# Kernel optimization log

Measured on AMD Instinct MI355X. Metric: run time of the kernel, lower is better.

The kernel has to match this reference:

```python
import jax, jax.numpy as jnp
import numpy as np

N_HEADS, INPUT_DIM, EMBED_DIM = 8, 512, 512
KEY_DIM = EMBED_DIM // N_HEADS  # val_dim == key_dim == 64


def _uniform(key, shape, stdv):
    return jax.random.uniform(key, shape, jnp.float32, -stdv, stdv)


def setup_inputs() -> dict:
    key = jax.random.key(0)
    kh, kq, kk, kv, ko = jax.random.split(key, 5)
    stdv_qkv = 1.0 / np.sqrt(KEY_DIM)
    stdv_out = 1.0 / np.sqrt(EMBED_DIM)
    return {
        "h": jax.random.normal(kh, (4, 2048, INPUT_DIM), jnp.float32),
        "W_query": _uniform(kq, (N_HEADS, INPUT_DIM, KEY_DIM), stdv_qkv),
        "W_key": _uniform(kk, (N_HEADS, INPUT_DIM, KEY_DIM), stdv_qkv),
        "W_val": _uniform(kv, (N_HEADS, INPUT_DIM, KEY_DIM), stdv_qkv),
        "W_out": _uniform(ko, (N_HEADS * KEY_DIM, EMBED_DIM), stdv_out),
    }


def reference(h, W_query, W_key, W_val, W_out):
    # h: [b, n, d_in]; W_{q,k,v}: [H, d_in, dk]; W_out: [H*dk, d_model]
    norm = 1.0 / np.sqrt(KEY_DIM)
    Q = jnp.einsum('bnd,hdk->hbnk', h, W_query)
    K = jnp.einsum('bnd,hdk->hbnk', h, W_key)
    V = jnp.einsum('bnd,hdk->hbnk', h, W_val)
    compat = norm * jnp.einsum('hbnk,hbmk->hbnm', Q, K)  # [H,b,n,n]
    attn = jax.nn.softmax(compat, axis=-1)
    heads = jnp.einsum('hbnm,hbmk->hbnk', attn, V)        # [H,b,n,dk]
    b, n = h.shape[0], h.shape[1]
    heads = jnp.transpose(heads, (1, 2, 0, 3)).reshape(b, n, N_HEADS * KEY_DIM)
    return heads @ W_out
```

## Files before the change

### kernel.cpp

```cpp
#include <hip/hip_runtime.h>
#include <hip/hip_bf16.h>
#include <hip/hip_fp16.h>

#define H 8
#define B 4
#define NSEQ 2048
#define DIN 512
#define DK 64
#define DMODEL 512
#define ROWS (B*NSEQ)

typedef _Float16 f16x8 __attribute__((ext_vector_type(8)));
typedef _Float16 f16x4 __attribute__((ext_vector_type(4)));
typedef float f32x4 __attribute__((ext_vector_type(4)));

#define EXP2F(x) __builtin_amdgcn_exp2f(x)

#define AS1(p) ((const __attribute__((address_space(1))) void*)(const void*)(p))
#define AS3(p) ((__attribute__((address_space(3))) void*)(void*)(p))

__global__ void k_prep(const float* __restrict__ h,
                       const float* __restrict__ Wq,
                       const float* __restrict__ Wk,
                       const float* __restrict__ Wv,
                       const float* __restrict__ Wo,
                       _Float16* __restrict__ hb,
                       _Float16* __restrict__ Wt,
                       _Float16* __restrict__ Wot)
{
    const long nh = (long)ROWS * DIN;
    const long nw = (long)3 * H * DK * DIN;
    const long no = (long)DMODEL * DMODEL;
    const long total = nh + nw + no;
    for (long i = (long)blockIdx.x * blockDim.x + threadIdx.x; i < total;
         i += (long)gridDim.x * blockDim.x) {
        if (i < nh) {
            hb[i] = (_Float16)h[i];
        } else if (i < nh + nw) {
            int j = (int)(i - nh);
            int m   = j / (H * DK * DIN);
            int rem = j % (H * DK * DIN);
            int hh  = rem / (DK * DIN);
            int r2  = rem % (DK * DIN);
            int c   = r2 / DIN;
            int d   = r2 % DIN;
            const float* W = (m == 0) ? Wq : ((m == 1) ? Wk : Wv);
            Wt[j] = (_Float16)W[hh * DIN * DK + d * DK + c];
        } else {
            int j = (int)(i - nh - nw);
            int e = j / DMODEL;
            int c = j % DMODEL;
            Wot[j] = (_Float16)Wo[c * DMODEL + e];
        }
    }
}

__global__ __launch_bounds__(256, 4) void k_qkv(
    const _Float16* __restrict__ hb,
    const _Float16* __restrict__ Wt,
    _Float16* __restrict__ Qs,
    _Float16* __restrict__ Kb,
    _Float16* __restrict__ Vt)
{
    const int rt = blockIdx.x;
    const int ct = blockIdx.y;
    const int t  = threadIdx.x;
    const int w  = t >> 6;
    const int l  = t & 63;
    const int l15 = l & 15, lg = l >> 4;
    const int wr = w >> 1, wc = w & 1;

    __shared__ _Float16 Al[2][128*32];
    __shared__ _Float16 Bl[2][128*32];

    const int srow  = l >> 2;
    const int schnk = (l & 3) ^ (srow & 3);
    const _Float16* asrc = hb + (long)(rt*128 + w*16 + srow)*DIN + schnk*8;
    const _Float16* bsrc = Wt + (long)(ct*128 + w*16 + srow)*DIN + schnk*8;

    auto stage = [&](int kt, int bufi) {
        const _Float16* as = asrc + kt*32;
        const _Float16* bs = bsrc + kt*32;
        __builtin_amdgcn_global_load_lds(AS1(as),          AS3(&Al[bufi][w*512]),        16, 0, 0);
        __builtin_amdgcn_global_load_lds(AS1(as + 64*DIN), AS3(&Al[bufi][2048 + w*512]), 16, 0, 0);
        __builtin_amdgcn_global_load_lds(AS1(bs),          AS3(&Bl[bufi][w*512]),        16, 0, 0);
        __builtin_amdgcn_global_load_lds(AS1(bs + 64*DIN), AS3(&Bl[bufi][2048 + w*512]), 16, 0, 0);
    };

    f32x4 acc[4][4] = {};

    stage(0, 0);
    __syncthreads();

    const int co = (lg ^ (l15 & 3)) * 8;
    for (int kt = 0; kt < 16; ++kt) {
        const int cur = kt & 1;
        if (kt + 1 < 16) stage(kt + 1, cur ^ 1);

        f16x8 af[4], bf[4];
#pragma unroll
        for (int am = 0; am < 4; ++am)
            af[am] = *(const f16x8*)&Al[cur][(wr*64 + am*16 + l15)*32 + co];
#pragma unroll
        for (int an = 0; an < 4; ++an)
            bf[an] = *(const f16x8*)&Bl[cur][(wc*64 + an*16 + l15)*32 + co];
#pragma unroll
        for (int am = 0; am < 4; ++am)
#pragma unroll
            for (int an = 0; an < 4; ++an)
                acc[am][an] = __builtin_amdgcn_mfma_f32_16x16x32_f16(af[am], bf[an], acc[am][an], 0, 0, 0);

        __syncthreads();
    }

    const int m = (ct*128) >> 9;
    const float QSCALE = 0.125f * 1.44269504088896f;
#pragma unroll
    for (int an = 0; an < 4; ++an) {
        const int col = ct*128 + wc*64 + an*16 + l15;
        const int hd = (col >> 6) & 7, dk = col & 63;
#pragma unroll
        for (int am = 0; am < 4; ++am) {
            const int rowb = rt*128 + wr*64 + am*16 + lg*4;
            const int b = rowb >> 11, n = rowb & 2047;
            const long p = (long)hd*B + b;
            if (m == 0) {
#pragma unroll
                for (int r = 0; r < 4; ++r)
                    Qs[(p*NSEQ + n + r)*DK + dk] = (_Float16)(acc[am][an][r] * QSCALE);
            } else if (m == 1) {
#pragma unroll
                for (int r = 0; r < 4; ++r)
                    Kb[(p*NSEQ + n + r)*DK + dk] = (_Float16)acc[am][an][r];
            } else {
                f16x4 pk;
                pk[0] = (_Float16)acc[am][an][0]; pk[1] = (_Float16)acc[am][an][1];
                pk[2] = (_Float16)acc[am][an][2]; pk[3] = (_Float16)acc[am][an][3];
                *(f16x4*)&Vt[(p*DK + dk)*NSEQ + n] = pk;
            }
        }
    }
}

__global__ __launch_bounds__(256, 2) void k_attn(
    const _Float16* __restrict__ Qs,
    const _Float16* __restrict__ Kb,
    const _Float16* __restrict__ Vt,
    _Float16* __restrict__ heads)
{
    const int bid = blockIdx.x;
    const int xcd = bid & 7, slot = bid >> 3;
    const int p   = (xcd << 2) | (slot >> 4);
    const int qt  = slot & 15;
    const int t = threadIdx.x, w = t >> 6, l = t & 63;
    const int l15 = l & 15, lg = l >> 4;

    __shared__ _Float16 Kl[2][64][64];
    __shared__ _Float16 Vl[2][64][64];
    __shared__ _Float16 Plds[4][2][16][64];

    const _Float16* Qp = Qs + (long)p*NSEQ*DK;
    const _Float16* Kp = Kb + (long)p*NSEQ*DK;
    const _Float16* Vp = Vt + (long)p*DK*NSEQ;

    const int qrow = qt*128 + w*32;
    f16x8 qa[2][2];
#pragma unroll
    for (int G = 0; G < 2; ++G) {
        qa[G][0] = *(const f16x8*)(Qp + (long)(qrow + G*16 + l15)*DK + 8*lg);
        qa[G][1] = *(const f16x8*)(Qp + (long)(qrow + G*16 + l15)*DK + 32 + 8*lg);
    }

    float mrun[2] = {-1e30f, -1e30f}, lrun[2] = {0.f, 0.f};
    f32x4 acco[2][4] = {};

    const int rsub = l >> 3;
    const int csw  = (l & 7) ^ rsub;
    auto stage = [&](int kt, int bufi) {
        const long kb = (long)kt * 64;
        __builtin_amdgcn_global_load_lds(
            AS1(Kp + (kb + w*16     + rsub)*DK + csw*8),
            AS3(&Kl[bufi][w*16][0]),     16, 0, 0);
        __builtin_amdgcn_global_load_lds(
            AS1(Kp + (kb + w*16 + 8 + rsub)*DK + csw*8),
            AS3(&Kl[bufi][w*16 + 8][0]), 16, 0, 0);
        __builtin_amdgcn_global_load_lds(
            AS1(Vp + (long)(w*16     + rsub)*NSEQ + kb + csw*8),
            AS3(&Vl[bufi][w*16][0]),     16, 0, 0);
        __builtin_amdgcn_global_load_lds(
            AS1(Vp + (long)(w*16 + 8 + rsub)*NSEQ + kb + csw*8),
            AS3(&Vl[bufi][w*16 + 8][0]), 16, 0, 0);
    };

    stage(0, 0);
    __syncthreads();

    for (int kt = 0; kt < 32; ++kt) {
        const int cur = kt & 1;
        if (kt + 1 < 32) stage(kt + 1, cur ^ 1);

        const char* kbase = (const char*)&Kl[cur][0][0];
        f16x8 kf[8];
#pragma unroll
        for (int f = 0; f < 4; ++f) {
            const int row = f*16 + l15;
            const int sw  = l15 & 7;
            kf[f*2]   = *(const f16x8*)(kbase + row*128 + ((lg     ^ sw)*16));
            kf[f*2+1] = *(const f16x8*)(kbase + row*128 + (((4+lg) ^ sw)*16));
        }

        f32x4 st[2][4] = {};
#pragma unroll
        for (int f = 0; f < 4; ++f)
#pragma unroll
            for (int G = 0; G < 2; ++G) {
                st[G][f] = __builtin_amdgcn_mfma_f32_16x16x32_f16(kf[f*2],   qa[G][0], st[G][f], 0, 0, 0);
                st[G][f] = __builtin_amdgcn_mfma_f32_16x16x32_f16(kf[f*2+1], qa[G][1], st[G][f], 0, 0, 0);
            }

        float mx[2];
#pragma unroll
        for (int G = 0; G < 2; ++G) {
            float mf[4];
#pragma unroll
            for (int f = 0; f < 4; ++f)
                mf[f] = fmaxf(fmaxf(st[G][f][0], st[G][f][1]), fmaxf(st[G][f][2], st[G][f][3]));
            float m0 = fmaxf(fmaxf(mf[0], mf[1]), fmaxf(mf[2], mf[3]));
            m0 = fmaxf(m0, __shfl_xor(m0, 16));
            m0 = fmaxf(m0, __shfl_xor(m0, 32));
            mx[G] = m0;
        }
        const bool skip = __all((mx[0] <= mrun[0] + 8.f) && (mx[1] <= mrun[1] + 8.f));
        if (!skip) {
#pragma unroll
            for (int G = 0; G < 2; ++G) {
                const float mnew = fmaxf(mrun[G], mx[G]);
                const float corr = EXP2F(mrun[G] - mnew);
                lrun[G] *= corr;
                mrun[G] = mnew;
#pragma unroll
                for (int r = 0; r < 4; ++r) {
                    const float cr = __shfl(corr, lg*4 + r);
#pragma unroll
                    for (int g = 0; g < 4; ++g) acco[G][g][r] *= cr;
                }
            }
        }
#pragma unroll
        for (int G = 0; G < 2; ++G) {
            float sf[4];
#pragma unroll
            for (int f = 0; f < 4; ++f) {
#pragma unroll
                for (int r = 0; r < 4; ++r) st[G][f][r] = EXP2F(st[G][f][r] - mrun[G]);
                sf[f] = (st[G][f][0] + st[G][f][1]) + (st[G][f][2] + st[G][f][3]);
            }
            float sum = (sf[0] + sf[1]) + (sf[2] + sf[3]);
            sum += __shfl_xor(sum, 16);
            sum += __shfl_xor(sum, 32);
            lrun[G] += sum;
        }

#pragma unroll
        for (int G = 0; G < 2; ++G) {
            char* pbase = (char*)&Plds[w][G][0][0];
#pragma unroll
            for (int f = 0; f < 4; ++f) {
                f16x4 pk;
                pk[0] = (_Float16)st[G][f][0]; pk[1] = (_Float16)st[G][f][1];
                pk[2] = (_Float16)st[G][f][2]; pk[3] = (_Float16)st[G][f][3];
                const int chnk = (f*2 + (lg >> 1)) ^ (l15 & 7);
                *(f16x4*)(pbase + l15*128 + chnk*16 + (lg & 1)*8) = pk;
            }
        }

        const char* vbase = (const char*)&Vl[cur][0][0];
        const char* pb0 = (const char*)&Plds[w][0][0][0];
        const char* pb1 = (const char*)&Plds[w][1][0][0];
#pragma unroll
        for (int kk = 0; kk < 2; ++kk) {
            const int pco = ((kk*4 + lg) ^ (l15 & 7)) * 16;
            f16x8 pa0 = *(const f16x8*)(pb0 + l15*128 + pco);
            f16x8 pa1 = *(const f16x8*)(pb1 + l15*128 + pco);
#pragma unroll
            for (int g = 0; g < 4; ++g) {
                const int row = g*16 + l15;
                f16x8 vf = *(const f16x8*)(vbase + row*128 + (((kk*4 + lg) ^ (l15 & 7))*16));
                acco[0][g] = __builtin_amdgcn_mfma_f32_16x16x32_f16(pa0, vf, acco[0][g], 0, 0, 0);
                acco[1][g] = __builtin_amdgcn_mfma_f32_16x16x32_f16(pa1, vf, acco[1][g], 0, 0, 0);
            }
        }

        __syncthreads();
    }

    const int hd = p >> 2, b = p & 3;
#pragma unroll
    for (int G = 0; G < 2; ++G) {
        const int rbase = qrow + G*16 + lg*4;
#pragma unroll
        for (int r = 0; r < 4; ++r) {
            const float inv = 1.f / __shfl(lrun[G], lg*4 + r);
            const int n = rbase + r;
            const long rowoff = ((long)b*NSEQ + n)*DMODEL + hd*64;
#pragma unroll
            for (int g = 0; g < 4; ++g)
                heads[rowoff + g*16 + l15] = (_Float16)(acco[G][g][r] * inv);
        }
    }
}

__global__ __launch_bounds__(256, 4) void k_out(
    const _Float16* __restrict__ heads,
    const _Float16* __restrict__ Wot,
    float* __restrict__ out)
{
    const int rt = blockIdx.x;
    const int ct = blockIdx.y;
    const int t = threadIdx.x, w = t >> 6, l = t & 63;
    const int l15 = l & 15, lg = l >> 4;
    const int wr = w >> 1, wc = w & 1;

    __shared__ _Float16 Al[2][128*32];
    __shared__ _Float16 Bl[2][128*32];

    const int srow  = l >> 2;
    const int schnk = (l & 3) ^ (srow & 3);
    const _Float16* asrc = heads + (long)(rt*128 + w*16 + srow)*DMODEL + schnk*8;
    const _Float16* bsrc = Wot   + (long)(ct*128 + w*16 + srow)*DMODEL + schnk*8;

    auto stage = [&](int kt, int bufi) {
        const _Float16* as = asrc + kt*32;
        const _Float16* bs = bsrc + kt*32;
        __builtin_amdgcn_global_load_lds(AS1(as),             AS3(&Al[bufi][w*512]),        16, 0, 0);
        __builtin_amdgcn_global_load_lds(AS1(as + 64*DMODEL), AS3(&Al[bufi][2048 + w*512]), 16, 0, 0);
        __builtin_amdgcn_global_load_lds(AS1(bs),             AS3(&Bl[bufi][w*512]),        16, 0, 0);
        __builtin_amdgcn_global_load_lds(AS1(bs + 64*DMODEL), AS3(&Bl[bufi][2048 + w*512]), 16, 0, 0);
    };

    f32x4 acc[4][4] = {};

    stage(0, 0);
    __syncthreads();

    const int co = (lg ^ (l15 & 3)) * 8;
    for (int kt = 0; kt < 16; ++kt) {
        const int cur = kt & 1;
        if (kt + 1 < 16) stage(kt + 1, cur ^ 1);

        f16x8 af[4], bf[4];
#pragma unroll
        for (int am = 0; am < 4; ++am)
            af[am] = *(const f16x8*)&Al[cur][(wr*64 + am*16 + l15)*32 + co];
#pragma unroll
        for (int an = 0; an < 4; ++an)
            bf[an] = *(const f16x8*)&Bl[cur][(wc*64 + an*16 + l15)*32 + co];
#pragma unroll
        for (int am = 0; am < 4; ++am)
#pragma unroll
            for (int an = 0; an < 4; ++an)
                acc[am][an] = __builtin_amdgcn_mfma_f32_16x16x32_f16(af[am], bf[an], acc[am][an], 0, 0, 0);

        __syncthreads();
    }

#pragma unroll
    for (int an = 0; an < 4; ++an) {
        const int col = ct*128 + wc*64 + an*16 + l15;
#pragma unroll
        for (int am = 0; am < 4; ++am) {
            const int rowb = rt*128 + wr*64 + am*16 + lg*4;
#pragma unroll
            for (int r = 0; r < 4; ++r)
                out[(long)(rowb + r)*DMODEL + col] = acc[am][an][r];
        }
    }
}

extern "C" void kernel_launch(void* const* d_in, const int* in_sizes, int n_in,
                              void* d_out, int out_size, void* d_ws, size_t ws_size,
                              hipStream_t stream) {
    const float* h  = (const float*)d_in[0];
    const float* Wq = (const float*)d_in[1];
    const float* Wk = (const float*)d_in[2];
    const float* Wv = (const float*)d_in[3];
    const float* Wo = (const float*)d_in[4];
    float* out = (float*)d_out;

    char* ws = (char*)d_ws;
    _Float16* hb    = (_Float16*)ws;  ws += (size_t)ROWS*DIN*2;
    _Float16* Wt    = (_Float16*)ws;  ws += (size_t)3*H*DK*DIN*2;
    _Float16* Wot   = (_Float16*)ws;  ws += (size_t)DMODEL*DMODEL*2;
    _Float16* Qs    = (_Float16*)ws;  ws += (size_t)H*B*NSEQ*DK*2;
    _Float16* Kb    = (_Float16*)ws;  ws += (size_t)H*B*NSEQ*DK*2;
    _Float16* Vt    = (_Float16*)ws;  ws += (size_t)H*B*NSEQ*DK*2;
    _Float16* heads = hb;

    k_prep<<<dim3(1024), dim3(256), 0, stream>>>(h, Wq, Wk, Wv, Wo, hb, Wt, Wot);
    k_qkv <<<dim3(64, 12), dim3(256), 0, stream>>>(hb, Wt, Qs, Kb, Vt);
    k_attn<<<dim3(512),    dim3(256), 0, stream>>>(Qs, Kb, Vt, heads);
    k_out <<<dim3(64, 4),  dim3(256), 0, stream>>>(heads, Wot, out);
}
```

Measured before the change: 109.5 us.

## Keep P in registers via permuted V layout and widen KV tile to 128

```diff
diff --git a/kernel.cpp b/kernel.cpp
--- a/kernel.cpp
+++ b/kernel.cpp
@@ -13,11 +13,17 @@
 typedef _Float16 f16x8 __attribute__((ext_vector_type(8)));
 typedef _Float16 f16x4 __attribute__((ext_vector_type(4)));
 typedef float f32x4 __attribute__((ext_vector_type(4)));
+typedef unsigned u32x4 __attribute__((ext_vector_type(4)));
 
 #define EXP2F(x) __builtin_amdgcn_exp2f(x)
 
 #define AS1(p) ((const __attribute__((address_space(1))) void*)(const void*)(p))
 #define AS3(p) ((__attribute__((address_space(3))) void*)(void*)(p))
+
+static __device__ __forceinline__ unsigned pk16(float a, float b) {
+    auto h = __builtin_amdgcn_cvt_pkrtz(a, b);
+    return __builtin_bit_cast(unsigned, h);
+}
 
 __global__ void k_prep(const float* __restrict__ h,
                        const float* __restrict__ Wq,
@@ -133,10 +139,13 @@
                 for (int r = 0; r < 4; ++r)
                     Kb[(p*NSEQ + n + r)*DK + dk] = (_Float16)acc[am][an][r];
             } else {
+                const int u0 = n & 127;
+                const int fu = u0 >> 4, lgu = (u0 >> 2) & 3;
+                const int tcol = (n & ~127) + (fu & 3)*32 + lgu*8 + (fu >> 2)*4;
                 f16x4 pk;
                 pk[0] = (_Float16)acc[am][an][0]; pk[1] = (_Float16)acc[am][an][1];
                 pk[2] = (_Float16)acc[am][an][2]; pk[3] = (_Float16)acc[am][an][3];
-                *(f16x4*)&Vt[(p*DK + dk)*NSEQ + n] = pk;
+                *(f16x4*)&Vt[(p*DK + dk)*NSEQ + tcol] = pk;
             }
         }
     }
@@ -155,9 +164,8 @@
     const int t = threadIdx.x, w = t >> 6, l = t & 63;
     const int l15 = l & 15, lg = l >> 4;
 
-    __shared__ _Float16 Kl[2][64][64];
-    __shared__ _Float16 Vl[2][64][64];
-    __shared__ _Float16 Plds[4][2][16][64];
+    __shared__ _Float16 Kl[2][128][64];
+    __shared__ _Float16 Vl[2][64][128];
 
     const _Float16* Qp = Qs + (long)p*NSEQ*DK;
     const _Float16* Kp = Kb + (long)p*NSEQ*DK;
@@ -174,58 +182,53 @@
     float mrun[2] = {-1e30f, -1e30f}, lrun[2] = {0.f, 0.f};
     f32x4 acco[2][4] = {};
 
-    const int rsub = l >> 3;
-    const int csw  = (l & 7) ^ rsub;
     auto stage = [&](int kt, int bufi) {
-        const long kb = (long)kt * 64;
-        __builtin_amdgcn_global_load_lds(
-            AS1(Kp + (kb + w*16     + rsub)*DK + csw*8),
-            AS3(&Kl[bufi][w*16][0]),     16, 0, 0);
-        __builtin_amdgcn_global_load_lds(
-            AS1(Kp + (kb + w*16 + 8 + rsub)*DK + csw*8),
-            AS3(&Kl[bufi][w*16 + 8][0]), 16, 0, 0);
-        __builtin_amdgcn_global_load_lds(
-            AS1(Vp + (long)(w*16     + rsub)*NSEQ + kb + csw*8),
-            AS3(&Vl[bufi][w*16][0]),     16, 0, 0);
-        __builtin_amdgcn_global_load_lds(
-            AS1(Vp + (long)(w*16 + 8 + rsub)*NSEQ + kb + csw*8),
-            AS3(&Vl[bufi][w*16 + 8][0]), 16, 0, 0);
+        const long kb = (long)kt * 128;
+#pragma unroll
+        for (int gi = 0; gi < 4; ++gi) {
+            const int krow = w*32 + gi*8 + (l >> 3);
+            const int kch  = (l & 7) ^ (krow & 7);
+            __builtin_amdgcn_global_load_lds(
+                AS1(Kp + (kb + krow)*DK + kch*8),
+                AS3(&Kl[bufi][w*32 + gi*8][0]), 16, 0, 0);
+            const int vrow = w*16 + gi*4 + (l >> 4);
+            const int vch  = (l & 15) ^ (vrow & 7);
+            __builtin_amdgcn_global_load_lds(
+                AS1(Vp + (long)vrow*NSEQ + kb + vch*8),
+                AS3(&Vl[bufi][w*16 + gi*4][0]), 16, 0, 0);
+        }
     };
 
     stage(0, 0);
     __syncthreads();
 
-    for (int kt = 0; kt < 32; ++kt) {
+    for (int kt = 0; kt < 16; ++kt) {
         const int cur = kt & 1;
-        if (kt + 1 < 32) stage(kt + 1, cur ^ 1);
+        if (kt + 1 < 16) stage(kt + 1, cur ^ 1);
 
         const char* kbase = (const char*)&Kl[cur][0][0];
-        f16x8 kf[8];
-#pragma unroll
-        for (int f = 0; f < 4; ++f) {
+        f32x4 st[2][8] = {};
+#pragma unroll
+        for (int f = 0; f < 8; ++f) {
             const int row = f*16 + l15;
             const int sw  = l15 & 7;
-            kf[f*2]   = *(const f16x8*)(kbase + row*128 + ((lg     ^ sw)*16));
-            kf[f*2+1] = *(const f16x8*)(kbase + row*128 + (((4+lg) ^ sw)*16));
-        }
-
-        f32x4 st[2][4] = {};
-#pragma unroll
-        for (int f = 0; f < 4; ++f)
-#pragma unroll
-            for (int G = 0; G < 2; ++G) {
-                st[G][f] = __builtin_amdgcn_mfma_f32_16x16x32_f16(kf[f*2],   qa[G][0], st[G][f], 0, 0, 0);
-                st[G][f] = __builtin_amdgcn_mfma_f32_16x16x32_f16(kf[f*2+1], qa[G][1], st[G][f], 0, 0, 0);
-            }
+            f16x8 k0 = *(const f16x8*)(kbase + row*128 + ((lg     ^ sw)*16));
+            f16x8 k1 = *(const f16x8*)(kbase + row*128 + (((4+lg) ^ sw)*16));
+            st[0][f] = __builtin_amdgcn_mfma_f32_16x16x32_f16(k0, qa[0][0], st[0][f], 0, 0, 0);
+            st[0][f] = __builtin_amdgcn_mfma_f32_16x16x32_f16(k1, qa[0][1], st[0][f], 0, 0, 0);
+            st[1][f] = __builtin_amdgcn_mfma_f32_16x16x32_f16(k0, qa[1][0], st[1][f], 0, 0, 0);
+            st[1][f] = __builtin_amdgcn_mfma_f32_16x16x32_f16(k1, qa[1][1], st[1][f], 0, 0, 0);
+        }
 
         float mx[2];
 #pragma unroll
         for (int G = 0; G < 2; ++G) {
-            float mf[4];
-#pragma unroll
-            for (int f = 0; f < 4; ++f)
+            float mf[8];
+#pragma unroll
+            for (int f = 0; f < 8; ++f)
                 mf[f] = fmaxf(fmaxf(st[G][f][0], st[G][f][1]), fmaxf(st[G][f][2], st[G][f][3]));
-            float m0 = fmaxf(fmaxf(mf[0], mf[1]), fmaxf(mf[2], mf[3]));
+            float m0 = fmaxf(fmaxf(fmaxf(mf[0], mf[1]), fmaxf(mf[2], mf[3])),
+                             fmaxf(fmaxf(mf[4], mf[5]), fmaxf(mf[6], mf[7])));
             m0 = fmaxf(m0, __shfl_xor(m0, 16));
             m0 = fmaxf(m0, __shfl_xor(m0, 32));
             mx[G] = m0;
@@ -248,44 +251,42 @@
         }
 #pragma unroll
         for (int G = 0; G < 2; ++G) {
-            float sf[4];
-#pragma unroll
-            for (int f = 0; f < 4; ++f) {
+            float sf[8];
+#pragma unroll
+            for (int f = 0; f < 8; ++f) {
 #pragma unroll
                 for (int r = 0; r < 4; ++r) st[G][f][r] = EXP2F(st[G][f][r] - mrun[G]);
                 sf[f] = (st[G][f][0] + st[G][f][1]) + (st[G][f][2] + st[G][f][3]);
             }
-            float sum = (sf[0] + sf[1]) + (sf[2] + sf[3]);
+            float sum = ((sf[0] + sf[1]) + (sf[2] + sf[3])) + ((sf[4] + sf[5]) + (sf[6] + sf[7]));
             sum += __shfl_xor(sum, 16);
             sum += __shfl_xor(sum, 32);
             lrun[G] += sum;
         }
 
-#pragma unroll
-        for (int G = 0; G < 2; ++G) {
-            char* pbase = (char*)&Plds[w][G][0][0];
-#pragma unroll
-            for (int f = 0; f < 4; ++f) {
-                f16x4 pk;
-                pk[0] = (_Float16)st[G][f][0]; pk[1] = (_Float16)st[G][f][1];
-                pk[2] = (_Float16)st[G][f][2]; pk[3] = (_Float16)st[G][f][3];
-                const int chnk = (f*2 + (lg >> 1)) ^ (l15 & 7);
-                *(f16x4*)(pbase + l15*128 + chnk*16 + (lg & 1)*8) = pk;
+        u32x4 paw[2][4];
+#pragma unroll
+        for (int G = 0; G < 2; ++G)
+#pragma unroll
+            for (int kk = 0; kk < 4; ++kk) {
+                u32x4 v4;
+                v4[0] = pk16(st[G][kk][0],   st[G][kk][1]);
+                v4[1] = pk16(st[G][kk][2],   st[G][kk][3]);
+                v4[2] = pk16(st[G][kk+4][0], st[G][kk+4][1]);
+                v4[3] = pk16(st[G][kk+4][2], st[G][kk+4][3]);
+                paw[G][kk] = v4;
             }
-        }
 
         const char* vbase = (const char*)&Vl[cur][0][0];
-        const char* pb0 = (const char*)&Plds[w][0][0][0];
-        const char* pb1 = (const char*)&Plds[w][1][0][0];
-#pragma unroll
-        for (int kk = 0; kk < 2; ++kk) {
-            const int pco = ((kk*4 + lg) ^ (l15 & 7)) * 16;
-            f16x8 pa0 = *(const f16x8*)(pb0 + l15*128 + pco);
-            f16x8 pa1 = *(const f16x8*)(pb1 + l15*128 + pco);
+#pragma unroll
+        for (int kk = 0; kk < 4; ++kk) {
+            const f16x8 pa0 = __builtin_bit_cast(f16x8, paw[0][kk]);
+            const f16x8 pa1 = __builtin_bit_cast(f16x8, paw[1][kk]);
 #pragma unroll
             for (int g = 0; g < 4; ++g) {
                 const int row = g*16 + l15;
-                f16x8 vf = *(const f16x8*)(vbase + row*128 + (((kk*4 + lg) ^ (l15 & 7))*16));
+                const int ch  = (kk*4 + lg) ^ (l15 & 7);
+                f16x8 vf = *(const f16x8*)(vbase + row*256 + ch*16);
                 acco[0][g] = __builtin_amdgcn_mfma_f32_16x16x32_f16(pa0, vf, acco[0][g], 0, 0, 0);
                 acco[1][g] = __builtin_amdgcn_mfma_f32_16x16x32_f16(pa1, vf, acco[1][g], 0, 0, 0);
             }
```

New measurement: 101.5 us. 7.3% less time.
